# Performance work log

Hardware: AMD Instinct MI355X
Metric: run time of the kernel (lower is better)

## Reference

```python
import jax, jax.numpy as jnp
import numpy as np

CAPACITY_FACTOR = 1.0  # fairseq Top1Gate default


def setup_inputs() -> dict:
    key = jax.random.key(0)
    ks = jax.random.split(key, 5)
    B, T, M, H, O, E = 8, 1024, 1024, 4096, 1024, 4
    return {
        "hidden_states": jax.random.normal(ks[0], (B, T, M), jnp.float32),
        "gate_w": jax.random.normal(ks[1], (M, E), jnp.float32) * 0.02,
        "fc1_w": jax.random.normal(ks[2], (E, M, H), jnp.float32) * 0.02,
        "fc1_b": jnp.zeros((E, H), jnp.float32),
        "fc2_w": jax.random.normal(ks[3], (E, H, O), jnp.float32) * 0.02,
        "fc2_b": jnp.zeros((E, O), jnp.float32),
    }


def reference(hidden_states, gate_w, fc1_w, fc1_b, fc2_w, fc2_b):
    B, T, M = hidden_states.shape
    E = gate_w.shape[1]
    S = B * T
    C = int(CAPACITY_FACTOR * -(-S // E))  # ceil(S/E)

    features = hidden_states.reshape(S, M)  # [S, M]

    # ---- Top1 gate (fairseq top1gating, eval path: no shuffle/noise) ----
    logits = features @ gate_w                      # [S, E]
    gates = jax.nn.softmax(logits, axis=1)          # [S, E]
    idx = jnp.argmax(gates, axis=1)                 # [S]
    mask1 = jax.nn.one_hot(idx, E, dtype=gates.dtype)  # [S, E]

    # load-balancing aux loss (computed before capacity dropping)
    me = jnp.mean(gates, axis=0)
    ce = jnp.mean(mask1, axis=0)
    l_aux = jnp.sum(me * ce) * E

    # capacity: position within each expert's queue; drop overflow tokens
    locations = jnp.cumsum(mask1, axis=0) - 1.0     # [S, E]
    mask1 = mask1 * (locations < C)
    loc_s = jnp.sum(locations * mask1, axis=1).astype(jnp.int32)  # [S]
    gates1_s = jnp.sum(gates * mask1, axis=1)       # [S] gate value (0 if dropped)

    # combine_weights [S, E, C] and boolean dispatch mask (as float for mm)
    combine = (gates1_s[:, None, None] * mask1[:, :, None]
               * jax.nn.one_hot(loc_s, C, dtype=gates.dtype)[:, None, :])
    dispatch = (combine > 0).astype(features.dtype)  # [S, E, C]

    # ---- dispatch via dense one-hot matmul: [E*C, S] @ [S, M] ----
    dispatch_ecs = jnp.transpose(dispatch, (1, 2, 0)).reshape(E * C, S)
    dispatched = (dispatch_ecs @ features).reshape(E, C, M)

    # ---- per-expert MLP (grouped GEMM) ----
    h = jax.nn.gelu(jnp.einsum('ecm,emh->ech', dispatched, fc1_w) + fc1_b[:, None, :])
    expert_out = jnp.einsum('ech,eho->eco', h, fc2_w) + fc2_b[:, None, :]  # [E, C, O]

    # ---- combine via dense matmul: [S, E*C] @ [E*C, O] ----
    O = expert_out.shape[-1]
    combined = combine.reshape(S, E * C) @ expert_out.reshape(E * C, O)

    return combined.reshape(B, T, O), l_aux
```

## Files before the change

### kernel.cpp

```cpp
#include <hip/hip_runtime.h>
#include <stdint.h>

#define S_TOK 8192
#define MDIM  1024
#define HDIM  4096
#define ODIM  1024
#define NEXP  4
#define CAP   2048

typedef __attribute__((ext_vector_type(8))) short short8;
typedef __attribute__((ext_vector_type(4))) float floatx4;

__device__ __forceinline__ unsigned short f2bf(float x) {
  union { float f; unsigned u; } v; v.f = x;
  unsigned r = v.u + 0x7FFFu + ((v.u >> 16) & 1u);
  return (unsigned short)(r >> 16);
}

__device__ __forceinline__ void gl_lds16(const void* g, void* l) {
  __builtin_amdgcn_global_load_lds(
      (const __attribute__((address_space(1))) void*)g,
      (__attribute__((address_space(3))) void*)l, 16, 0, 0);
}

__device__ __forceinline__ float gelu_tanh(float x) {
  float z = 0.7978845608028654f * (x + 0.044715f * x * x * x);
  float t = 1.0f - 2.0f / (__expf(2.0f * z) + 1.0f);
  return 0.5f * x * (1.0f + t);
}

__global__ __launch_bounds__(256) void gate_kernel(
    const float* __restrict__ feat, const float* __restrict__ gw,
    int* __restrict__ idx, float* __restrict__ gval, float* __restrict__ gsum)
{
  int wave = threadIdx.x >> 6, lane = threadIdx.x & 63;
  int s = blockIdx.x * 4 + wave;
  const float* f = feat + (size_t)s * MDIM;
  double a0 = 0, a1 = 0, a2 = 0, a3 = 0;
  #pragma unroll
  for (int j = 0; j < 16; ++j) {
    int m = lane + j * 64;
    float x = f[m];
    float4 w = ((const float4*)gw)[m];
    a0 += (double)x * w.x; a1 += (double)x * w.y;
    a2 += (double)x * w.z; a3 += (double)x * w.w;
  }
  #pragma unroll
  for (int off = 32; off; off >>= 1) {
    a0 += __shfl_down(a0, off); a1 += __shfl_down(a1, off);
    a2 += __shfl_down(a2, off); a3 += __shfl_down(a3, off);
  }
  __shared__ float bs[4];
  if (threadIdx.x < 4) bs[threadIdx.x] = 0.f;
  __syncthreads();
  if (lane == 0) {
    double lg[4] = {a0, a1, a2, a3};
    double mx = lg[0]; int bi = 0;
    #pragma unroll
    for (int e = 1; e < 4; ++e) if (lg[e] > mx) { mx = lg[e]; bi = e; }
    float ex[4]; float den = 0.f;
    #pragma unroll
    for (int e = 0; e < 4; ++e) { ex[e] = __expf((float)(lg[e] - mx)); den += ex[e]; }
    float inv = 1.f / den;
    idx[s]  = bi;
    gval[s] = ex[bi] * inv;
    #pragma unroll
    for (int e = 0; e < 4; ++e) atomicAdd(&bs[e], ex[e] * inv);
  }
  __syncthreads();
  if (threadIdx.x < 4) atomicAdd(&gsum[threadIdx.x], bs[threadIdx.x]);
}

__global__ void scan_kernel(const int* __restrict__ idx, int* __restrict__ perm,
                            int* __restrict__ ne, const float* __restrict__ gsum,
                            float* __restrict__ laux)
{
  int lane = threadIdx.x;
  unsigned long long below = (lane == 0) ? 0ull : ((~0ull) >> (64 - lane));
  int off[4] = {0, 0, 0, 0};
  for (int base = 0; base < S_TOK; base += 512) {
    int v[8];
    #pragma unroll
    for (int j = 0; j < 8; ++j) v[j] = idx[base + j * 64 + lane];
    #pragma unroll
    for (int j = 0; j < 8; ++j) {
      int myE = v[j];
      int s = base + j * 64 + lane;
      #pragma unroll
      for (int e = 0; e < 4; ++e) {
        unsigned long long mb = __ballot(myE == e);
        if (myE == e) {
          int rank = off[e] + __popcll(mb & below);
          if (rank < CAP) perm[e * CAP + rank] = s;
        }
        off[e] += __popcll(mb);
      }
    }
  }
  if (lane < 4) ne[lane] = off[lane] < CAP ? off[lane] : CAP;
  if (lane == 0) {
    float l = 0.f;
    #pragma unroll
    for (int e = 0; e < 4; ++e)
      l += (gsum[e] * (1.0f / S_TOK)) * ((float)off[e] * (1.0f / S_TOK));
    *laux = l * (float)NEXP;
  }
}

__global__ __launch_bounds__(256) void transpose_cast(
    const float* __restrict__ in, unsigned short* __restrict__ out, int R, int Cc)
{
  __shared__ unsigned short tile[64][66];
  in  += (size_t)blockIdx.z * R * Cc;
  out += (size_t)blockIdx.z * R * Cc;
  int c0 = blockIdx.x * 64, r0 = blockIdx.y * 64;
  int tx = threadIdx.x & 15;
  int ty = threadIdx.x >> 4;
  #pragma unroll
  for (int p = 0; p < 4; ++p) {
    int r = ty + p * 16;
    float4 v = *(const float4*)(in + (size_t)(r0 + r) * Cc + c0 + tx * 4);
    tile[r][tx * 4 + 0] = f2bf(v.x);
    tile[r][tx * 4 + 1] = f2bf(v.y);
    tile[r][tx * 4 + 2] = f2bf(v.z);
    tile[r][tx * 4 + 3] = f2bf(v.w);
  }
  __syncthreads();
  #pragma unroll
  for (int p = 0; p < 4; ++p) {
    int c = ty + p * 16;
    ushort4 o;
    o.x = tile[tx * 4 + 0][c];
    o.y = tile[tx * 4 + 1][c];
    o.z = tile[tx * 4 + 2][c];
    o.w = tile[tx * 4 + 3][c];
    *(ushort4*)(out + (size_t)(c0 + c) * R + r0 + tx * 4) = o;
  }
}

__global__ __launch_bounds__(256) void gather_kernel(
    const float* __restrict__ feat, const int* __restrict__ perm,
    const int* __restrict__ ne, unsigned short* __restrict__ disp)
{
  int b = blockIdx.x;
  int e = b >> 11, c = b & (CAP - 1);
  int m = threadIdx.x * 4;
  ushort4 o;
  if (c < ne[e]) {
    int s = perm[b];
    float4 v = *(const float4*)(feat + (size_t)s * MDIM + m);
    o.x = f2bf(v.x); o.y = f2bf(v.y); o.z = f2bf(v.z); o.w = f2bf(v.w);
  } else {
    o.x = o.y = o.z = o.w = 0;
  }
  *(ushort4*)(disp + (size_t)b * MDIM + m) = o;
}

__global__ __launch_bounds__(256) void fc1_kernel(
    const unsigned short* __restrict__ A, const unsigned short* __restrict__ Bt,
    const float* __restrict__ b1, unsigned short* __restrict__ Hb)
{
  const int e = blockIdx.z, nb = blockIdx.x, mb = blockIdx.y;
  const int tid = threadIdx.x, wave = tid >> 6, lane = tid & 63;

  __shared__ __align__(16) unsigned short smA[128 * 32];
  __shared__ __align__(16) unsigned short smB[128 * 32];

  const char* Ag = (const char*)(A + ((size_t)e * CAP + (size_t)mb * 128) * MDIM);
  const char* Bg = (const char*)(Bt + ((size_t)e * HDIM + (size_t)nb * 128) * MDIM);

  int boff0 = (wave * 2 + 0) * 1024 + lane * 16;
  int boff1 = (wave * 2 + 1) * 1024 + lane * 16;
  const char* agp0 = Ag + (size_t)(boff0 >> 6) * 2048 + (boff0 & 63);
  const char* agp1 = Ag + (size_t)(boff1 >> 6) * 2048 + (boff1 & 63);
  const char* bgp0 = Bg + (size_t)(boff0 >> 6) * 2048 + (boff0 & 63);
  const char* bgp1 = Bg + (size_t)(boff1 >> 6) * 2048 + (boff1 & 63);
  unsigned short* sA0 = smA + (wave * 2 + 0) * 512;
  unsigned short* sA1 = smA + (wave * 2 + 1) * 512;
  unsigned short* sB0 = smB + (wave * 2 + 0) * 512;
  unsigned short* sB1 = smB + (wave * 2 + 1) * 512;

  const int wm = (wave & 1) * 64, wn = (wave >> 1) * 64;
  const int fr = lane & 15, fq = lane >> 4;

  floatx4 acc[4][4] = {};

  for (int kt = 0; kt < MDIM / 32; ++kt) {
    int kb = kt * 64;
    gl_lds16(agp0 + kb, sA0);
    gl_lds16(agp1 + kb, sA1);
    gl_lds16(bgp0 + kb, sB0);
    gl_lds16(bgp1 + kb, sB1);
    __syncthreads();
    short8 af[4], bfr[4];
    #pragma unroll
    for (int i = 0; i < 4; ++i)
      af[i] = *(const short8*)&smA[(wm + i * 16 + fr) * 32 + fq * 8];
    #pragma unroll
    for (int j = 0; j < 4; ++j)
      bfr[j] = *(const short8*)&smB[(wn + j * 16 + fr) * 32 + fq * 8];
    #pragma unroll
    for (int i = 0; i < 4; ++i)
      #pragma unroll
      for (int j = 0; j < 4; ++j)
        acc[i][j] = __builtin_amdgcn_mfma_f32_16x16x32_bf16(af[i], bfr[j], acc[i][j], 0, 0, 0);
    __syncthreads();
  }

  unsigned short* Hrow = Hb + (size_t)e * CAP * HDIM;
  #pragma unroll
  for (int j = 0; j < 4; ++j) {
    int gn = nb * 128 + wn + j * 16 + fr;
    float bv = b1[e * HDIM + gn];
    #pragma unroll
    for (int i = 0; i < 4; ++i) {
      int m0 = mb * 128 + wm + i * 16 + fq * 4;
      #pragma unroll
      for (int r = 0; r < 4; ++r)
        Hrow[(size_t)(m0 + r) * HDIM + gn] = f2bf(gelu_tanh(acc[i][j][r] + bv));
    }
  }
}

__global__ __launch_bounds__(256) void fc2_kernel(
    const unsigned short* __restrict__ A, const unsigned short* __restrict__ Bt,
    const float* __restrict__ b2, const int* __restrict__ perm,
    const int* __restrict__ ne, const float* __restrict__ gval,
    float* __restrict__ out)
{
  const int e = blockIdx.z, nb = blockIdx.x, mb = blockIdx.y;
  const int tid = threadIdx.x, wave = tid >> 6, lane = tid & 63;

  __shared__ __align__(16) unsigned short smA[128 * 32];
  __shared__ __align__(16) unsigned short smB[128 * 32];

  const char* Ag = (const char*)(A + ((size_t)e * CAP + (size_t)mb * 128) * HDIM);
  const char* Bg = (const char*)(Bt + ((size_t)e * ODIM + (size_t)nb * 128) * HDIM);

  int boff0 = (wave * 2 + 0) * 1024 + lane * 16;
  int boff1 = (wave * 2 + 1) * 1024 + lane * 16;
  const char* agp0 = Ag + (size_t)(boff0 >> 6) * 8192 + (boff0 & 63);
  const char* agp1 = Ag + (size_t)(boff1 >> 6) * 8192 + (boff1 & 63);
  const char* bgp0 = Bg + (size_t)(boff0 >> 6) * 8192 + (boff0 & 63);
  const char* bgp1 = Bg + (size_t)(boff1 >> 6) * 8192 + (boff1 & 63);
  unsigned short* sA0 = smA + (wave * 2 + 0) * 512;
  unsigned short* sA1 = smA + (wave * 2 + 1) * 512;
  unsigned short* sB0 = smB + (wave * 2 + 0) * 512;
  unsigned short* sB1 = smB + (wave * 2 + 1) * 512;

  const int wm = (wave & 1) * 64, wn = (wave >> 1) * 64;
  const int fr = lane & 15, fq = lane >> 4;

  floatx4 acc[4][4] = {};

  for (int kt = 0; kt < HDIM / 32; ++kt) {
    int kb = kt * 64;
    gl_lds16(agp0 + kb, sA0);
    gl_lds16(agp1 + kb, sA1);
    gl_lds16(bgp0 + kb, sB0);
    gl_lds16(bgp1 + kb, sB1);
    __syncthreads();
    short8 af[4], bfr[4];
    #pragma unroll
    for (int i = 0; i < 4; ++i)
      af[i] = *(const short8*)&smA[(wm + i * 16 + fr) * 32 + fq * 8];
    #pragma unroll
    for (int j = 0; j < 4; ++j)
      bfr[j] = *(const short8*)&smB[(wn + j * 16 + fr) * 32 + fq * 8];
    #pragma unroll
    for (int i = 0; i < 4; ++i)
      #pragma unroll
      for (int j = 0; j < 4; ++j)
        acc[i][j] = __builtin_amdgcn_mfma_f32_16x16x32_bf16(af[i], bfr[j], acc[i][j], 0, 0, 0);
    __syncthreads();
  }

  const int nE = ne[e];
  float b2v[4];
  #pragma unroll
  for (int j = 0; j < 4; ++j)
    b2v[j] = b2[e * ODIM + nb * 128 + wn + j * 16 + fr];
  #pragma unroll
  for (int i = 0; i < 4; ++i) {
    #pragma unroll
    for (int r = 0; r < 4; ++r) {
      int c = mb * 128 + wm + i * 16 + fq * 4 + r;
      if (c < nE) {
        int s = perm[e * CAP + c];
        float g = gval[s];
        float* orow = out + (size_t)s * ODIM + nb * 128 + wn;
        #pragma unroll
        for (int j = 0; j < 4; ++j)
          orow[j * 16 + fr] = (acc[i][j][r] + b2v[j]) * g;
      }
    }
  }
}

extern "C" void kernel_launch(void* const* d_in, const int* in_sizes, int n_in,
                              void* d_out, int out_size, void* d_ws, size_t ws_size,
                              hipStream_t stream) {
  const float* feat = (const float*)d_in[0];
  const float* gw   = (const float*)d_in[1];
  const float* w1   = (const float*)d_in[2];
  const float* b1   = (const float*)d_in[3];
  const float* w2   = (const float*)d_in[4];
  const float* b2   = (const float*)d_in[5];
  float* out = (float*)d_out;

  char* ws = (char*)d_ws;
  unsigned short* wt   = (unsigned short*)(ws);
  unsigned short* hbuf = (unsigned short*)(ws + 33554432);
  unsigned short* disp = (unsigned short*)(ws + 100663296);
  int*   idx  = (int*)  (ws + 117440512);
  float* gval = (float*)(ws + 117473280);
  int*   perm = (int*)  (ws + 117506048);
  float* gsum = (float*)(ws + 117538816);
  int*   ne   = (int*)  (ws + 117538832);

  hipMemsetAsync(d_out, 0, (size_t)S_TOK * ODIM * sizeof(float), stream);
  hipMemsetAsync(ws + 117538816, 0, 32, stream);

  gate_kernel<<<S_TOK / 4, 256, 0, stream>>>(feat, gw, idx, gval, gsum);
  scan_kernel<<<1, 64, 0, stream>>>(idx, perm, ne, gsum, out + (size_t)S_TOK * ODIM);
  transpose_cast<<<dim3(HDIM / 64, MDIM / 64, NEXP), 256, 0, stream>>>(w1, wt, MDIM, HDIM);
  gather_kernel<<<NEXP * CAP, 256, 0, stream>>>(feat, perm, ne, disp);
  fc1_kernel<<<dim3(HDIM / 128, CAP / 128, NEXP), 256, 0, stream>>>(disp, wt, b1, hbuf);
  transpose_cast<<<dim3(ODIM / 64, HDIM / 64, NEXP), 256, 0, stream>>>(w2, wt, HDIM, ODIM);
  fc2_kernel<<<dim3(ODIM / 128, CAP / 128, NEXP), 256, 0, stream>>>(hbuf, wt, b2, perm, ne, gval, out);
}
```

Before: 477.6 us.

## Double-buffer LDS tiles in fc1 and fc2 GEMM kernels

```diff
diff --git a/kernel.cpp b/kernel.cpp
--- a/kernel.cpp
+++ b/kernel.cpp
@@ -163,8 +163,8 @@
   const int e = blockIdx.z, nb = blockIdx.x, mb = blockIdx.y;
   const int tid = threadIdx.x, wave = tid >> 6, lane = tid & 63;
 
-  __shared__ __align__(16) unsigned short smA[128 * 32];
-  __shared__ __align__(16) unsigned short smB[128 * 32];
+  __shared__ __align__(16) unsigned short smA[2][128 * 32];
+  __shared__ __align__(16) unsigned short smB[2][128 * 32];
 
   const char* Ag = (const char*)(A + ((size_t)e * CAP + (size_t)mb * 128) * MDIM);
   const char* Bg = (const char*)(Bt + ((size_t)e * HDIM + (size_t)nb * 128) * MDIM);
@@ -175,36 +175,44 @@
   const char* agp1 = Ag + (size_t)(boff1 >> 6) * 2048 + (boff1 & 63);
   const char* bgp0 = Bg + (size_t)(boff0 >> 6) * 2048 + (boff0 & 63);
   const char* bgp1 = Bg + (size_t)(boff1 >> 6) * 2048 + (boff1 & 63);
-  unsigned short* sA0 = smA + (wave * 2 + 0) * 512;
-  unsigned short* sA1 = smA + (wave * 2 + 1) * 512;
-  unsigned short* sB0 = smB + (wave * 2 + 0) * 512;
-  unsigned short* sB1 = smB + (wave * 2 + 1) * 512;
+  const int so0 = (wave * 2 + 0) * 512;
+  const int so1 = (wave * 2 + 1) * 512;
 
   const int wm = (wave & 1) * 64, wn = (wave >> 1) * 64;
   const int fr = lane & 15, fq = lane >> 4;
 
   floatx4 acc[4][4] = {};
 
+  {
+    gl_lds16(agp0, &smA[0][so0]);
+    gl_lds16(agp1, &smA[0][so1]);
+    gl_lds16(bgp0, &smB[0][so0]);
+    gl_lds16(bgp1, &smB[0][so1]);
+  }
+  int cur = 0;
   for (int kt = 0; kt < MDIM / 32; ++kt) {
-    int kb = kt * 64;
-    gl_lds16(agp0 + kb, sA0);
-    gl_lds16(agp1 + kb, sA1);
-    gl_lds16(bgp0 + kb, sB0);
-    gl_lds16(bgp1 + kb, sB1);
     __syncthreads();
+    if (kt + 1 < MDIM / 32) {
+      int kb = (kt + 1) * 64;
+      int nx = cur ^ 1;
+      gl_lds16(agp0 + kb, &smA[nx][so0]);
+      gl_lds16(agp1 + kb, &smA[nx][so1]);
+      gl_lds16(bgp0 + kb, &smB[nx][so0]);
+      gl_lds16(bgp1 + kb, &smB[nx][so1]);
+    }
     short8 af[4], bfr[4];
     #pragma unroll
     for (int i = 0; i < 4; ++i)
-      af[i] = *(const short8*)&smA[(wm + i * 16 + fr) * 32 + fq * 8];
+      af[i] = *(const short8*)&smA[cur][(wm + i * 16 + fr) * 32 + fq * 8];
     #pragma unroll
     for (int j = 0; j < 4; ++j)
-      bfr[j] = *(const short8*)&smB[(wn + j * 16 + fr) * 32 + fq * 8];
+      bfr[j] = *(const short8*)&smB[cur][(wn + j * 16 + fr) * 32 + fq * 8];
     #pragma unroll
     for (int i = 0; i < 4; ++i)
       #pragma unroll
       for (int j = 0; j < 4; ++j)
         acc[i][j] = __builtin_amdgcn_mfma_f32_16x16x32_bf16(af[i], bfr[j], acc[i][j], 0, 0, 0);
-    __syncthreads();
+    cur ^= 1;
   }
 
   unsigned short* Hrow = Hb + (size_t)e * CAP * HDIM;
@@ -231,8 +239,8 @@
   const int e = blockIdx.z, nb = blockIdx.x, mb = blockIdx.y;
   const int tid = threadIdx.x, wave = tid >> 6, lane = tid & 63;
 
-  __shared__ __align__(16) unsigned short smA[128 * 32];
-  __shared__ __align__(16) unsigned short smB[128 * 32];
+  __shared__ __align__(16) unsigned short smA[2][128 * 32];
+  __shared__ __align__(16) unsigned short smB[2][128 * 32];
 
   const char* Ag = (const char*)(A + ((size_t)e * CAP + (size_t)mb * 128) * HDIM);
   const char* Bg = (const char*)(Bt + ((size_t)e * ODIM + (size_t)nb * 128) * HDIM);
@@ -243,36 +251,44 @@
   const char* agp1 = Ag + (size_t)(boff1 >> 6) * 8192 + (boff1 & 63);
   const char* bgp0 = Bg + (size_t)(boff0 >> 6) * 8192 + (boff0 & 63);
   const char* bgp1 = Bg + (size_t)(boff1 >> 6) * 8192 + (boff1 & 63);
-  unsigned short* sA0 = smA + (wave * 2 + 0) * 512;
-  unsigned short* sA1 = smA + (wave * 2 + 1) * 512;
-  unsigned short* sB0 = smB + (wave * 2 + 0) * 512;
-  unsigned short* sB1 = smB + (wave * 2 + 1) * 512;
+  const int so0 = (wave * 2 + 0) * 512;
+  const int so1 = (wave * 2 + 1) * 512;
 
   const int wm = (wave & 1) * 64, wn = (wave >> 1) * 64;
   const int fr = lane & 15, fq = lane >> 4;
 
   floatx4 acc[4][4] = {};
 
+  {
+    gl_lds16(agp0, &smA[0][so0]);
+    gl_lds16(agp1, &smA[0][so1]);
+    gl_lds16(bgp0, &smB[0][so0]);
+    gl_lds16(bgp1, &smB[0][so1]);
+  }
+  int cur = 0;
   for (int kt = 0; kt < HDIM / 32; ++kt) {
-    int kb = kt * 64;
-    gl_lds16(agp0 + kb, sA0);
-    gl_lds16(agp1 + kb, sA1);
-    gl_lds16(bgp0 + kb, sB0);
-    gl_lds16(bgp1 + kb, sB1);
     __syncthreads();
+    if (kt + 1 < HDIM / 32) {
+      int kb = (kt + 1) * 64;
+      int nx = cur ^ 1;
+      gl_lds16(agp0 + kb, &smA[nx][so0]);
+      gl_lds16(agp1 + kb, &smA[nx][so1]);
+      gl_lds16(bgp0 + kb, &smB[nx][so0]);
+      gl_lds16(bgp1 + kb, &smB[nx][so1]);
+    }
     short8 af[4], bfr[4];
     #pragma unroll
     for (int i = 0; i < 4; ++i)
-      af[i] = *(const short8*)&smA[(wm + i * 16 + fr) * 32 + fq * 8];
+      af[i] = *(const short8*)&smA[cur][(wm + i * 16 + fr) * 32 + fq * 8];
     #pragma unroll
     for (int j = 0; j < 4; ++j)
-      bfr[j] = *(const short8*)&smB[(wn + j * 16 + fr) * 32 + fq * 8];
+      bfr[j] = *(const short8*)&smB[cur][(wn + j * 16 + fr) * 32 + fq * 8];
     #pragma unroll
     for (int i = 0; i < 4; ++i)
       #pragma unroll
       for (int j = 0; j < 4; ++j)
         acc[i][j] = __builtin_amdgcn_mfma_f32_16x16x32_bf16(af[i], bfr[j], acc[i][j], 0, 0, 0);
-    __syncthreads();
+    cur ^= 1;
   }
 
   const int nE = ne[e];
```

Result: slower. 493.6 us (+3.3%).

## Parallelize expert scan across 16 waves and halve fc2 M-tile for more blocks

Applied to the files above, without the earlier changes.

```diff
diff --git a/kernel.cpp b/kernel.cpp
--- a/kernel.cpp
+++ b/kernel.cpp
@@ -71,38 +71,57 @@
   if (threadIdx.x < 4) atomicAdd(&gsum[threadIdx.x], bs[threadIdx.x]);
 }
 
-__global__ void scan_kernel(const int* __restrict__ idx, int* __restrict__ perm,
-                            int* __restrict__ ne, const float* __restrict__ gsum,
-                            float* __restrict__ laux)
-{
-  int lane = threadIdx.x;
+__global__ __launch_bounds__(1024) void scan_kernel(
+    const int* __restrict__ idx, int* __restrict__ perm,
+    int* __restrict__ ne, const float* __restrict__ gsum,
+    float* __restrict__ laux)
+{
+  const int tid = threadIdx.x, wave = tid >> 6, lane = tid & 63;
+  __shared__ int cnt[16][4];
+  __shared__ int off[16][4];
+  __shared__ int tot[4];
   unsigned long long below = (lane == 0) ? 0ull : ((~0ull) >> (64 - lane));
-  int off[4] = {0, 0, 0, 0};
-  for (int base = 0; base < S_TOK; base += 512) {
-    int v[8];
-    #pragma unroll
-    for (int j = 0; j < 8; ++j) v[j] = idx[base + j * 64 + lane];
-    #pragma unroll
-    for (int j = 0; j < 8; ++j) {
-      int myE = v[j];
-      int s = base + j * 64 + lane;
-      #pragma unroll
-      for (int e = 0; e < 4; ++e) {
-        unsigned long long mb = __ballot(myE == e);
-        if (myE == e) {
-          int rank = off[e] + __popcll(mb & below);
-          if (rank < CAP) perm[e * CAP + rank] = s;
-        }
-        off[e] += __popcll(mb);
-      }
+
+  int myE[8], loc[8];
+  int c[4] = {0, 0, 0, 0};
+  #pragma unroll
+  for (int j = 0; j < 8; ++j) {
+    int s = wave * 512 + j * 64 + lane;
+    int ev = idx[s];
+    myE[j] = ev;
+    #pragma unroll
+    for (int e = 0; e < 4; ++e) {
+      unsigned long long mb = __ballot(ev == e);
+      if (ev == e) loc[j] = c[e] + __popcll(mb & below);
+      c[e] += __popcll(mb);
     }
   }
-  if (lane < 4) ne[lane] = off[lane] < CAP ? off[lane] : CAP;
   if (lane == 0) {
+    #pragma unroll
+    for (int e = 0; e < 4; ++e) cnt[wave][e] = c[e];
+  }
+  __syncthreads();
+  if (tid < 64) {
+    int w = tid >> 2, e = tid & 3;
+    int o = 0;
+    for (int w2 = 0; w2 < 16; ++w2) if (w2 < w) o += cnt[w2][e];
+    off[w][e] = o;
+    if (w == 15) tot[e] = o + cnt[15][e];
+  }
+  __syncthreads();
+  #pragma unroll
+  for (int j = 0; j < 8; ++j) {
+    int s = wave * 512 + j * 64 + lane;
+    int e = myE[j];
+    int rank = off[wave][e] + loc[j];
+    if (rank < CAP) perm[e * CAP + rank] = s;
+  }
+  if (tid < 4) ne[tid] = tot[tid] < CAP ? tot[tid] : CAP;
+  if (tid == 0) {
     float l = 0.f;
     #pragma unroll
     for (int e = 0; e < 4; ++e)
-      l += (gsum[e] * (1.0f / S_TOK)) * ((float)off[e] * (1.0f / S_TOK));
+      l += (gsum[e] * (1.0f / S_TOK)) * ((float)tot[e] * (1.0f / S_TOK));
     *laux = l * (float)NEXP;
   }
 }
@@ -231,44 +250,42 @@
   const int e = blockIdx.z, nb = blockIdx.x, mb = blockIdx.y;
   const int tid = threadIdx.x, wave = tid >> 6, lane = tid & 63;
 
-  __shared__ __align__(16) unsigned short smA[128 * 32];
+  __shared__ __align__(16) unsigned short smA[64 * 32];
   __shared__ __align__(16) unsigned short smB[128 * 32];
 
-  const char* Ag = (const char*)(A + ((size_t)e * CAP + (size_t)mb * 128) * HDIM);
+  const char* Ag = (const char*)(A + ((size_t)e * CAP + (size_t)mb * 64) * HDIM);
   const char* Bg = (const char*)(Bt + ((size_t)e * ODIM + (size_t)nb * 128) * HDIM);
 
+  int boffA = tid * 16;
+  const char* agp = Ag + (size_t)(boffA >> 6) * 8192 + (boffA & 63);
+  unsigned short* sA = smA + wave * 512;
   int boff0 = (wave * 2 + 0) * 1024 + lane * 16;
   int boff1 = (wave * 2 + 1) * 1024 + lane * 16;
-  const char* agp0 = Ag + (size_t)(boff0 >> 6) * 8192 + (boff0 & 63);
-  const char* agp1 = Ag + (size_t)(boff1 >> 6) * 8192 + (boff1 & 63);
   const char* bgp0 = Bg + (size_t)(boff0 >> 6) * 8192 + (boff0 & 63);
   const char* bgp1 = Bg + (size_t)(boff1 >> 6) * 8192 + (boff1 & 63);
-  unsigned short* sA0 = smA + (wave * 2 + 0) * 512;
-  unsigned short* sA1 = smA + (wave * 2 + 1) * 512;
   unsigned short* sB0 = smB + (wave * 2 + 0) * 512;
   unsigned short* sB1 = smB + (wave * 2 + 1) * 512;
 
-  const int wm = (wave & 1) * 64, wn = (wave >> 1) * 64;
+  const int wm = (wave & 1) * 32, wn = (wave >> 1) * 64;
   const int fr = lane & 15, fq = lane >> 4;
 
-  floatx4 acc[4][4] = {};
+  floatx4 acc[2][4] = {};
 
   for (int kt = 0; kt < HDIM / 32; ++kt) {
     int kb = kt * 64;
-    gl_lds16(agp0 + kb, sA0);
-    gl_lds16(agp1 + kb, sA1);
+    gl_lds16(agp + kb, sA);
     gl_lds16(bgp0 + kb, sB0);
     gl_lds16(bgp1 + kb, sB1);
     __syncthreads();
-    short8 af[4], bfr[4];
-    #pragma unroll
-    for (int i = 0; i < 4; ++i)
+    short8 af[2], bfr[4];
+    #pragma unroll
+    for (int i = 0; i < 2; ++i)
       af[i] = *(const short8*)&smA[(wm + i * 16 + fr) * 32 + fq * 8];
     #pragma unroll
     for (int j = 0; j < 4; ++j)
       bfr[j] = *(const short8*)&smB[(wn + j * 16 + fr) * 32 + fq * 8];
     #pragma unroll
-    for (int i = 0; i < 4; ++i)
+    for (int i = 0; i < 2; ++i)
       #pragma unroll
       for (int j = 0; j < 4; ++j)
         acc[i][j] = __builtin_amdgcn_mfma_f32_16x16x32_bf16(af[i], bfr[j], acc[i][j], 0, 0, 0);
@@ -281,10 +298,10 @@
   for (int j = 0; j < 4; ++j)
     b2v[j] = b2[e * ODIM + nb * 128 + wn + j * 16 + fr];
   #pragma unroll
-  for (int i = 0; i < 4; ++i) {
+  for (int i = 0; i < 2; ++i) {
     #pragma unroll
     for (int r = 0; r < 4; ++r) {
-      int c = mb * 128 + wm + i * 16 + fq * 4 + r;
+      int c = mb * 64 + wm + i * 16 + fq * 4 + r;
       if (c < nE) {
         int s = perm[e * CAP + c];
         float g = gval[s];
@@ -322,10 +339,10 @@
   hipMemsetAsync(ws + 117538816, 0, 32, stream);
 
   gate_kernel<<<S_TOK / 4, 256, 0, stream>>>(feat, gw, idx, gval, gsum);
-  scan_kernel<<<1, 64, 0, stream>>>(idx, perm, ne, gsum, out + (size_t)S_TOK * ODIM);
+  scan_kernel<<<1, 1024, 0, stream>>>(idx, perm, ne, gsum, out + (size_t)S_TOK * ODIM);
   transpose_cast<<<dim3(HDIM / 64, MDIM / 64, NEXP), 256, 0, stream>>>(w1, wt, MDIM, HDIM);
   gather_kernel<<<NEXP * CAP, 256, 0, stream>>>(feat, perm, ne, disp);
   fc1_kernel<<<dim3(HDIM / 128, CAP / 128, NEXP), 256, 0, stream>>>(disp, wt, b1, hbuf);
   transpose_cast<<<dim3(ODIM / 64, HDIM / 64, NEXP), 256, 0, stream>>>(w2, wt, HDIM, ODIM);
-  fc2_kernel<<<dim3(ODIM / 128, CAP / 128, NEXP), 256, 0, stream>>>(hbuf, wt, b2, perm, ne, gval, out);
-}
+  fc2_kernel<<<dim3(ODIM / 128, CAP / 64, NEXP), 256, 0, stream>>>(hbuf, wt, b2, perm, ne, gval, out);
+}
```

New measurement: 441.1 us. 1.08x faster.
